# Kernel optimization log

Measured on AMD Instinct MI355X. Metric: run time of the kernel, lower is better.

Reference implementation:

```python
import jax, jax.numpy as jnp
import numpy as np
import math

D_MODEL = 1024
NUM_HEADS = 16
HEAD_DIM = D_MODEL // NUM_HEADS
BATCH = 2
SEQ = 2048
THETA = 10000.0


def _rope_tables(seq_len, head_dim, theta=THETA):
    inv_freq = 1.0 / theta ** (jnp.arange(0, head_dim, 2, dtype=jnp.float32) / head_dim)
    pos = jnp.arange(seq_len, dtype=jnp.float32)
    freqs = jnp.outer(pos, inv_freq)                 # [S, hd/2]
    emb = jnp.concatenate([freqs, freqs], axis=-1)   # [S, hd]
    return jnp.cos(emb), jnp.sin(emb)


def _rotate_half(x):
    x1, x2 = jnp.split(x, 2, axis=-1)
    return jnp.concatenate([-x2, x1], axis=-1)


def setup_inputs() -> dict:
    key = jax.random.key(0)
    k1, k2, k3 = jax.random.split(key, 3)
    x = jax.random.normal(k1, (BATCH, SEQ, D_MODEL), dtype=jnp.float32)
    # causal mask: 1 where attend allowed, 0 where masked
    mask = jnp.tril(jnp.ones((SEQ, SEQ), dtype=jnp.int32))[None, None]
    w_qkv = jax.random.normal(k2, (D_MODEL, 3 * D_MODEL), dtype=jnp.float32) / math.sqrt(D_MODEL)
    w_out = jax.random.normal(k3, (D_MODEL, D_MODEL), dtype=jnp.float32) / math.sqrt(D_MODEL)
    return {"x": x, "mask": mask, "w_qkv": w_qkv, "w_out": w_out}


def reference(x, mask, w_qkv, w_out):
    B, S, _ = x.shape
    qkv = x @ w_qkv                                          # [B,S,3*D]
    qkv = qkv.reshape(B, S, 3, NUM_HEADS, HEAD_DIM)
    qkv = jnp.transpose(qkv, (2, 0, 3, 1, 4))                # [3,B,H,S,hd]
    q, k, v = qkv[0], qkv[1], qkv[2]
    cos, sin = _rope_tables(S, HEAD_DIM)                     # [S,hd]
    cos = cos[None, None]; sin = sin[None, None]
    q = q * cos + _rotate_half(q) * sin
    k = k * cos + _rotate_half(k) * sin
    scores = jnp.einsum('bhqd,bhkd->bhqk', q, k) / math.sqrt(HEAD_DIM)
    scores = jnp.where(mask == 0, -jnp.inf, scores)
    attn = jax.nn.softmax(scores, axis=-1)                   # dropout p=0 (eval)
    out = jnp.einsum('bhqk,bhkd->bhqd', attn, v)             # [B,H,S,hd]
    out = jnp.transpose(out, (0, 2, 1, 3)).reshape(B, S, D_MODEL)
    return out @ w_out
```

## Files before the change

### kernel.cpp

```cpp
#include <hip/hip_runtime.h>

typedef __bf16 bf16;
typedef __bf16 bf16x4 __attribute__((ext_vector_type(4)));
typedef __bf16 bf16x8 __attribute__((ext_vector_type(8)));
typedef short s16x4 __attribute__((ext_vector_type(4)));
typedef float f32x4 __attribute__((ext_vector_type(4)));

constexpr int BATCH = 2;
constexpr int SEQ   = 2048;
constexpr int DMODEL= 1024;
constexpr int NH    = 16;
constexpr int HD    = 64;
constexpr int M_ROWS= BATCH * SEQ;
constexpr int N_QKV = 3 * DMODEL;

#if defined(__HIP_DEVICE_COMPILE__) && __has_builtin(__builtin_amdgcn_exp2f)
#define EXP2(x) __builtin_amdgcn_exp2f(x)
#else
#define EXP2(x) exp2f(x)
#endif

__device__ __forceinline__ void gl_lds16(const bf16* g, bf16* l) {
  __builtin_amdgcn_global_load_lds(
      (const __attribute__((address_space(1))) unsigned int*)g,
      (__attribute__((address_space(3))) unsigned int*)l, 16, 0, 0);
}

__device__ __forceinline__ f32x4 mfma_16x16x16_bf16(bf16x4 a, bf16x4 b,
                                                    f32x4 c) {
#if defined(__HIP_DEVICE_COMPILE__)
  union { bf16x4 h; s16x4 s; } ua{a}, ub{b};
  return __builtin_amdgcn_mfma_f32_16x16x16bf16_1k(ua.s, ub.s, c, 0, 0, 0);
#else
  return c;
#endif
}

__global__ __launch_bounds__(256) void prep_kernel(
    const float* __restrict__ x, const float* __restrict__ w_qkv,
    const float* __restrict__ w_out, bf16* __restrict__ xb,
    bf16* __restrict__ WqkvT, bf16* __restrict__ WoutT) {
  const int bx = blockIdx.x, t = threadIdx.x;
  if (bx < 2048) {
    const int i = (bx * 256 + t) * 8;
    float4 f0 = *(const float4*)&x[i];
    float4 f1 = *(const float4*)&x[i + 4];
    bf16x8 v;
    v[0] = (bf16)f0.x; v[1] = (bf16)f0.y; v[2] = (bf16)f0.z; v[3] = (bf16)f0.w;
    v[4] = (bf16)f1.x; v[5] = (bf16)f1.y; v[6] = (bf16)f1.z; v[7] = (bf16)f1.w;
    *(bf16x8*)&xb[i] = v;
    return;
  }
  __shared__ float tile[32][33];
  const float* src;
  bf16* dst;
  int R, C, c0, r0;
  if (bx < 5120) {
    const int idx = bx - 2048;
    src = w_qkv; dst = WqkvT; R = DMODEL; C = N_QKV;
    c0 = (idx % 96) * 32; r0 = (idx / 96) * 32;
  } else {
    const int idx = bx - 5120;
    src = w_out; dst = WoutT; R = DMODEL; C = DMODEL;
    c0 = (idx & 31) * 32; r0 = (idx >> 5) * 32;
  }
  const int r = t >> 3, c4 = (t & 7) * 4;
  {
    float4 f = *(const float4*)&src[(size_t)(r0 + r) * C + c0 + c4];
    tile[r][c4 + 0] = f.x; tile[r][c4 + 1] = f.y;
    tile[r][c4 + 2] = f.z; tile[r][c4 + 3] = f.w;
  }
  __syncthreads();
  {
    bf16x4 v;
#pragma unroll
    for (int j = 0; j < 4; j++) v[j] = (bf16)tile[c4 + j][r];
    *(bf16x4*)&dst[(size_t)(c0 + r) * R + r0 + c4] = v;
  }
}

__global__ __launch_bounds__(256) void gemm_out64(
    const bf16* __restrict__ A, const bf16* __restrict__ BT,
    float* __restrict__ C, int M, int N, int K) {
  __shared__ bf16 As[64 * 32];
  __shared__ bf16 Bs[128 * 32];
  const int t = threadIdx.x;
  const int m0 = blockIdx.y * 64;
  const int n0 = blockIdx.x * 128;
  const int w = t >> 6, lane = t & 63, g = lane >> 4, li = lane & 15;
  const int r0w = (w & 1) * 32, c0w = (w >> 1) * 64;
  f32x4 acc[2][4] = {};
  for (int k0 = 0; k0 < K; k0 += 32) {
    __syncthreads();
    {
      const int idx = w * 64 + lane;
      const int row = idx >> 2, col = (idx & 3) * 8;
      gl_lds16(&A[(size_t)(m0 + row) * K + k0 + col], &As[w * 512]);
    }
#pragma unroll
    for (int c = 0; c < 2; c++) {
      const int idx = (w * 2 + c) * 64 + lane;
      const int row = idx >> 2, col = (idx & 3) * 8;
      gl_lds16(&BT[(size_t)(n0 + row) * K + k0 + col], &Bs[(w * 2 + c) * 512]);
    }
    __syncthreads();
    bf16x8 a[2], b[4];
#pragma unroll
    for (int mt = 0; mt < 2; mt++)
      a[mt] = *(const bf16x8*)&As[(r0w + mt * 16 + li) * 32 + g * 8];
#pragma unroll
    for (int nt = 0; nt < 4; nt++)
      b[nt] = *(const bf16x8*)&Bs[(c0w + nt * 16 + li) * 32 + g * 8];
#pragma unroll
    for (int mt = 0; mt < 2; mt++)
#pragma unroll
      for (int nt = 0; nt < 4; nt++)
        acc[mt][nt] = __builtin_amdgcn_mfma_f32_16x16x32_bf16(
            a[mt], b[nt], acc[mt][nt], 0, 0, 0);
  }
#pragma unroll
  for (int mt = 0; mt < 2; mt++)
#pragma unroll
    for (int nt = 0; nt < 4; nt++)
#pragma unroll
      for (int r = 0; r < 4; r++) {
        const int m = m0 + r0w + mt * 16 + g * 4 + r;
        const int n = n0 + c0w + nt * 16 + li;
        C[(size_t)m * N + n] = acc[mt][nt][r];
      }
}

__global__ __launch_bounds__(256) void gemm_qkv_rope(
    const bf16* __restrict__ A, const bf16* __restrict__ BT,
    bf16* __restrict__ Qb, bf16* __restrict__ Kb, bf16* __restrict__ Vt) {
  constexpr int K = DMODEL;
  __shared__ bf16 smem[16384];
  const int t = threadIdx.x;
  const int m0 = blockIdx.y * 128;
  const int n0 = blockIdx.x * 128;
  const int w = t >> 6, lane = t & 63, g = lane >> 4, li = lane & 15;
  const int r0w = (w & 1) * 64, c0w = (w >> 1) * 64;
  f32x4 acc[4][4] = {};

  const int i0 = (w * 2 + 0) * 64 + lane, i1 = (w * 2 + 1) * 64 + lane;
  const int sr0 = i0 >> 2, sc0 = (i0 & 3) * 8;
  const int sr1 = i1 >> 2, sc1 = (i1 & 3) * 8;

#define QKV_STAGE(buf, k0)                                                   \
  {                                                                          \
    bf16* Asb = smem + (buf)*4096;                                           \
    bf16* Bsb = smem + 8192 + (buf)*4096;                                    \
    gl_lds16(&A[(size_t)(m0 + sr0) * K + (k0) + sc0],                        \
             &Asb[(w * 2 + 0) * 512]);                                       \
    gl_lds16(&A[(size_t)(m0 + sr1) * K + (k0) + sc1],                        \
             &Asb[(w * 2 + 1) * 512]);                                       \
    gl_lds16(&BT[(size_t)(n0 + sr0) * K + (k0) + sc0],                       \
             &Bsb[(w * 2 + 0) * 512]);                                       \
    gl_lds16(&BT[(size_t)(n0 + sr1) * K + (k0) + sc1],                       \
             &Bsb[(w * 2 + 1) * 512]);                                       \
  }

  QKV_STAGE(0, 0);
  __syncthreads();
  for (int it = 0; it < 32; ++it) {
    const int cur = it & 1;
    if (it < 31) QKV_STAGE(cur ^ 1, (it + 1) * 32);
    const bf16* Asb = smem + cur * 4096;
    const bf16* Bsb = smem + 8192 + cur * 4096;
    bf16x8 a[4], b[4];
#pragma unroll
    for (int mt = 0; mt < 4; mt++)
      a[mt] = *(const bf16x8*)&Asb[(r0w + mt * 16 + li) * 32 + g * 8];
#pragma unroll
    for (int nt = 0; nt < 4; nt++)
      b[nt] = *(const bf16x8*)&Bsb[(c0w + nt * 16 + li) * 32 + g * 8];
#pragma unroll
    for (int mt = 0; mt < 4; mt++)
#pragma unroll
      for (int nt = 0; nt < 4; nt++)
        acc[mt][nt] = __builtin_amdgcn_mfma_f32_16x16x32_bf16(
            a[mt], b[nt], acc[mt][nt], 0, 0, 0);
    __syncthreads();
  }
#undef QKV_STAGE

  const int region = n0 >> 10;
  const int b = m0 >> 11;
  const int h = ((n0 + c0w) >> 6) & 15;
  const size_t bh = (size_t)(b * NH + h);

  if (region < 2) {
    bf16* dst = region == 0 ? Qb : Kb;
    const float outsc = region == 0 ? 0.125f * 1.44269504f : 1.f;
    const float L = 13.287712379549449f;
    const float if0 = exp2f(-(float)(2 * li) / 64.f * L);
    const float if1 = exp2f(-(float)(2 * (li + 16)) / 64.f * L);
    bf16* lw = smem + w * 2112;
#pragma unroll
    for (int pass = 0; pass < 2; pass++) {
      __syncthreads();
#pragma unroll
      for (int mtl = 0; mtl < 2; mtl++) {
        const int mt = pass * 2 + mtl;
#pragma unroll
        for (int r = 0; r < 4; r++) {
          const int s = (m0 + r0w + mt * 16 + g * 4 + r) & (SEQ - 1);
          float cs[2], sn[2];
          __sincosf((float)s * if0, &sn[0], &cs[0]);
          __sincosf((float)s * if1, &sn[1], &cs[1]);
#pragma unroll
          for (int nt = 0; nt < 4; nt++) {
            const int par = nt & 1;
            const float a = acc[mt][nt][r];
            const float ap = acc[mt][nt ^ 2][r];
            const float v = (nt < 2) ? a * cs[par] - ap * sn[par]
                                     : a * cs[par] + ap * sn[par];
            lw[(mtl * 16 + g * 4 + r) * 66 + nt * 16 + li] =
                (bf16)(v * outsc);
          }
        }
      }
      __syncthreads();
      const int rowl = lane >> 1, dh = (lane & 1) * 32;
      const int s = (m0 + r0w + pass * 32 + rowl) & (SEQ - 1);
      bf16* gdst = &dst[(bh * SEQ + s) * HD + dh];
      const bf16* lsrc = &lw[rowl * 66 + dh];
#pragma unroll
      for (int c = 0; c < 4; c++)
        *(bf16x8*)&gdst[c * 8] = *(const bf16x8*)&lsrc[c * 8];
    }
  } else {
#pragma unroll
    for (int mt = 0; mt < 4; mt++)
#pragma unroll
      for (int nt = 0; nt < 4; nt++) {
        const int s = (m0 + r0w + mt * 16 + g * 4) & (SEQ - 1);
        const int d = nt * 16 + li;
        bf16x4 v;
#pragma unroll
        for (int r = 0; r < 4; r++) v[r] = (bf16)acc[mt][nt][r];
        *(bf16x4*)&Vt[(bh * HD + d) * SEQ + s] = v;
      }
  }
}

__device__ const unsigned char CHUNK_TAB[80] = {
    124, 125, 126, 127,
    120, 121, 122, 116, 117, 118, 112, 113, 114, 108, 109, 110,
    104, 105, 106, 100, 101, 102, 96,  97,  98,  92,  93,  94,
    88,  89,  84,  85,  80,  81,  76,  77,  72,  73,  68,  69,
    64,  65,  60,  61,
    56,  52,  48,  44,  40,  36,  32,  28,
    24,  57,  90,  123, 20,  53,  86,  119, 16,  49,  82,  115,
    12,  45,  78,  111, 8,   41,  74,  107, 4,   37,  70,  103,
    0,   33,  66,  99};

__global__ __launch_bounds__(256, 5) void flash_attn15(
    const bf16* __restrict__ Q, const bf16* __restrict__ Kb,
    const bf16* __restrict__ Vt, bf16* __restrict__ Oout,
    float* __restrict__ Opart, float* __restrict__ Lpart) {
  const int bx = blockIdx.x;
  const unsigned char e = CHUNK_TAB[bx >> 5];
  const int qt = e >> 2, kch = e & 3;
  const int bh = bx & 31;
  const int q0 = qt * 64;
  const int jlo = kch * 8;
  const int jhi = min(jlo + 8, qt + 1);
  const int t = threadIdx.x, w = t >> 6, lane = t & 63, g = lane >> 4,
            li = lane & 15;

  __shared__ bf16 Ks[2][4096];
  __shared__ bf16 Vs[2][4096];

  const bf16* Qh = Q  + (size_t)bh * SEQ * HD;
  const bf16* Kh = Kb + (size_t)bh * SEQ * HD;
  const bf16* Vh = Vt + (size_t)bh * HD * SEQ;

  const int qw = q0 + w * 16;

  bf16x8 qf[2];
#pragma unroll
  for (int ks = 0; ks < 2; ks++)
    qf[ks] = *(const bf16x8*)&Qh[(size_t)(qw + li) * HD + ks * 32 + g * 8];

  f32x4 o[4] = {};
  f32x4 o4  = {};
  bf16x4 ones;
#pragma unroll
  for (int r = 0; r < 4; r++) ones[r] = (bf16)1.f;

  int koffB[2][4];
#pragma unroll
  for (int ks = 0; ks < 2; ks++)
#pragma unroll
    for (int nt = 0; nt < 4; nt++) {
      const int rK = nt * 16 + li;
      const int pK = rK * 8 + ((ks * 4 + g) ^ (li & 7));
      koffB[ks][nt] = pK * 16;
    }
  int voffB[4][4];
#pragma unroll
  for (int nt = 0; nt < 4; nt++)
#pragma unroll
    for (int dt = 0; dt < 4; dt++) {
      const int rV = dt * 16 + li;
      const int cg = nt * 2 + (g >> 1);
      const int pV = rV * 8 + (cg ^ (rV & 7));
      voffB[nt][dt] = pV * 16 + (g & 1) * 8;
    }

  const int p0 = w * 128 + lane, p1 = p0 + 64;
  const int sr0 = p0 >> 3, sc0 = ((p0 & 7) ^ (sr0 & 7)) * 8;
  const int sr1 = p1 >> 3, sc1 = ((p1 & 7) ^ (sr1 & 7)) * 8;
  const int lo0 = w * 1024, lo1 = w * 1024 + 512;

  {
    const int jn = jlo * 64;
    gl_lds16(&Kh[(size_t)(jn + sr0) * HD + sc0], &Ks[jlo & 1][lo0]);
    gl_lds16(&Kh[(size_t)(jn + sr1) * HD + sc1], &Ks[jlo & 1][lo1]);
    gl_lds16(&Vh[(size_t)sr0 * SEQ + jn + sc0], &Vs[jlo & 1][lo0]);
    gl_lds16(&Vh[(size_t)sr1 * SEQ + jn + sc1], &Vs[jlo & 1][lo1]);
  }
  __syncthreads();

  for (int ti = jlo; ti < jhi; ++ti) {
    const int cur = ti & 1, nxt = cur ^ 1;
    const char* ksb = (const char*)&Ks[cur][0];
    const char* vsb = (const char*)&Vs[cur][0];
    if (ti + 1 < jhi) {
      const int jn = ti * 64 + 64;
      gl_lds16(&Kh[(size_t)(jn + sr0) * HD + sc0], &Ks[nxt][lo0]);
      gl_lds16(&Kh[(size_t)(jn + sr1) * HD + sc1], &Ks[nxt][lo1]);
      gl_lds16(&Vh[(size_t)sr0 * SEQ + jn + sc0], &Vs[nxt][lo0]);
      gl_lds16(&Vh[(size_t)sr1 * SEQ + jn + sc1], &Vs[nxt][lo1]);
    }

    if (ti < qt) {
      f32x4 sacc[4] = {};
      __builtin_amdgcn_s_setprio(1);
#pragma unroll
      for (int ks = 0; ks < 2; ks++)
#pragma unroll
        for (int nt = 0; nt < 4; nt++) {
          bf16x8 kf = *(const bf16x8*)(ksb + koffB[ks][nt]);
          sacc[nt] = __builtin_amdgcn_mfma_f32_16x16x32_bf16(kf, qf[ks],
                                                             sacc[nt], 0, 0, 0);
        }
      __builtin_amdgcn_s_setprio(0);

      bf16x4 pf[4];
#pragma unroll
      for (int nt = 0; nt < 4; nt++)
#pragma unroll
        for (int r = 0; r < 4; r++) pf[nt][r] = (bf16)EXP2(sacc[nt][r]);

      __builtin_amdgcn_s_setprio(1);
#pragma unroll
      for (int nt = 0; nt < 4; nt++) {
        o4 = mfma_16x16x16_bf16(ones, pf[nt], o4);
#pragma unroll
        for (int dt = 0; dt < 4; dt++) {
          bf16x4 vfrag = *(const bf16x4*)(vsb + voffB[nt][dt]);
          o[dt] = mfma_16x16x16_bf16(vfrag, pf[nt], o[dt]);
        }
      }
      __builtin_amdgcn_s_setprio(0);
    } else {
      f32x4 sacc[4] = {};
      __builtin_amdgcn_s_setprio(1);
#pragma unroll
      for (int ks = 0; ks < 2; ks++)
#pragma unroll
        for (int nt = 0; nt < 4; nt++) {
          if (nt > w) continue;
          bf16x8 kf = *(const bf16x8*)(ksb + koffB[ks][nt]);
          sacc[nt] = __builtin_amdgcn_mfma_f32_16x16x32_bf16(kf, qf[ks],
                                                             sacc[nt], 0, 0, 0);
        }
      __builtin_amdgcn_s_setprio(0);

      bf16x4 pf[4];
#pragma unroll
      for (int nt = 0; nt < 4; nt++) {
        if (nt > w) continue;
#pragma unroll
        for (int r = 0; r < 4; r++) {
          float v = sacc[nt][r];
          if (nt == w) {
            const int kk = nt * 16 + g * 4 + r;
            v = (kk <= w * 16 + li) ? v : -1e30f;
          }
          pf[nt][r] = (bf16)EXP2(v);
        }
      }

      __builtin_amdgcn_s_setprio(1);
#pragma unroll
      for (int nt = 0; nt < 4; nt++) {
        if (nt > w) continue;
        o4 = mfma_16x16x16_bf16(ones, pf[nt], o4);
#pragma unroll
        for (int dt = 0; dt < 4; dt++) {
          bf16x4 vfrag = *(const bf16x4*)(vsb + voffB[nt][dt]);
          o[dt] = mfma_16x16x16_bf16(vfrag, pf[nt], o[dt]);
        }
      }
      __builtin_amdgcn_s_setprio(0);
    }
    __syncthreads();
  }

  if (qt <= 7) {
    const float inv_l = 1.f / o4[0];
    const int b = bh >> 4, h = bh & 15;
    const int s = qw + li;
#pragma unroll
    for (int dt = 0; dt < 4; dt++) {
      bf16x4 ov;
#pragma unroll
      for (int r = 0; r < 4; r++) ov[r] = (bf16)(o[dt][r] * inv_l);
      *(bf16x4*)&Oout[((size_t)(b * SEQ + s)) * DMODEL + h * 64 + dt * 16 +
                      g * 4] = ov;
    }
  } else {
    const int s = qw + li;
    int off;
    if (qt < 16)       off = (s - 512) * 2 + kch;
    else if (qt < 24)  off = 1024 + (s - 1024) * 3 + kch;
    else               off = 2560 + (s - 1536) * 4 + kch;
    const size_t slot = (size_t)bh * 4608 + off;
    if (g == 0) Lpart[slot] = o4[0];
    float* od = &Opart[slot * 64];
#pragma unroll
    for (int dt = 0; dt < 4; dt++)
      *(f32x4*)&od[dt * 16 + g * 4] = o[dt];
  }
}

__global__ __launch_bounds__(256) void attn_merge2(
    const float* __restrict__ Opart, const float* __restrict__ Lpart,
    bf16* __restrict__ attn) {
  const int gi = blockIdx.x * 256 + threadIdx.x;
  const int row = gi >> 3;
  const int d0 = (gi & 7) * 8;
  const int bh = row / 1536, srel = row - bh * 1536;
  const int b = bh >> 4, h = bh & 15, s = srel + 512;
  int off0, nc;
  if (srel < 512)       { off0 = srel * 2;                nc = 2; }
  else if (srel < 1024) { off0 = 1024 + (srel - 512) * 3; nc = 3; }
  else                  { off0 = 2560 + (srel - 1024) * 4; nc = 4; }
  const size_t base = (size_t)bh * 4608 + off0;
  float lsum = 0.f;
  float acc[8] = {};
  for (int c = 0; c < nc; c++) {
    lsum += Lpart[base + c];
    const float* p = &Opart[(base + c) * 64 + d0];
    float4 a0 = *(const float4*)p;
    float4 a1 = *(const float4*)(p + 4);
    acc[0] += a0.x; acc[1] += a0.y; acc[2] += a0.z; acc[3] += a0.w;
    acc[4] += a1.x; acc[5] += a1.y; acc[6] += a1.z; acc[7] += a1.w;
  }
  const float inv = 1.f / lsum;
  bf16x8 v;
#pragma unroll
  for (int i = 0; i < 8; i++) v[i] = (bf16)(acc[i] * inv);
  *(bf16x8*)&attn[((size_t)(b * SEQ + s)) * DMODEL + h * 64 + d0] = v;
}

extern "C" void kernel_launch(void* const* d_in, const int* in_sizes, int n_in,
                              void* d_out, int out_size, void* d_ws,
                              size_t ws_size, hipStream_t stream) {
  const float* x     = (const float*)d_in[0];
  const float* w_qkv = (const float*)d_in[2];
  const float* w_out = (const float*)d_in[3];
  float* out = (float*)d_out;

  char* ws = (char*)d_ws;
  bf16* WqkvT = (bf16*)(ws);
  bf16* WoutT = (bf16*)(ws + 6291456);
  bf16* xb    = (bf16*)(ws + 8388608);
  bf16* Qb    = (bf16*)(ws + 16777216);
  bf16* Kbuf  = (bf16*)(ws + 25165824);
  bf16* Vt    = (bf16*)(ws + 33554432);
  bf16* attn  = (bf16*)(ws + 41943040);
  float* Opart= (float*)(ws + 50331648);
  float* Lpart= (float*)(ws + 88080384);

  prep_kernel<<<dim3(6144), 256, 0, stream>>>(x, w_qkv, w_out, xb, WqkvT,
                                              WoutT);
  gemm_qkv_rope<<<dim3(N_QKV / 128, M_ROWS / 128), 256, 0, stream>>>(
      xb, WqkvT, Qb, Kbuf, Vt);
  flash_attn15<<<dim3(2560), 256, 0, stream>>>(Qb, Kbuf, Vt, attn, Opart,
                                               Lpart);
  attn_merge2<<<dim3(1536), 256, 0, stream>>>(Opart, Lpart, attn);
  gemm_out64<<<dim3(DMODEL / 128, M_ROWS / 64), 256, 0, stream>>>(
      attn, WoutT, out, M_ROWS, DMODEL, DMODEL);
}
```

Baseline: 198.5 us.

## Fuse split-KV merge into flash attention via atomic ticket last-block reduction

Removes the separate attn_merge2 kernel. Each split-KV attention block now writes its partials, fences, and takes an atomic ticket per (head, q-tile); the last-arriving block sums the Lpart/Opart partials and writes the normalized bf16 output. The ticket counters are zeroed by an extra block in prep_kernel. This saves a kernel launch and lets the merge overlap with other attention blocks, at the cost of atomics, fences and a serialized tail reduction inside the attention kernel.

```diff
diff --git a/kernel.cpp b/kernel.cpp
--- a/kernel.cpp
+++ b/kernel.cpp
@@ -39,7 +39,8 @@
 __global__ __launch_bounds__(256) void prep_kernel(
     const float* __restrict__ x, const float* __restrict__ w_qkv,
     const float* __restrict__ w_out, bf16* __restrict__ xb,
-    bf16* __restrict__ WqkvT, bf16* __restrict__ WoutT) {
+    bf16* __restrict__ WqkvT, bf16* __restrict__ WoutT,
+    int* __restrict__ ticket) {
   const int bx = blockIdx.x, t = threadIdx.x;
   if (bx < 2048) {
     const int i = (bx * 256 + t) * 8;
@@ -49,6 +50,11 @@
     v[0] = (bf16)f0.x; v[1] = (bf16)f0.y; v[2] = (bf16)f0.z; v[3] = (bf16)f0.w;
     v[4] = (bf16)f1.x; v[5] = (bf16)f1.y; v[6] = (bf16)f1.z; v[7] = (bf16)f1.w;
     *(bf16x8*)&xb[i] = v;
+    return;
+  }
+  if (bx >= 6144) {
+    int4 z = {0, 0, 0, 0};
+    *(int4*)&ticket[t * 4] = z;
     return;
   }
   __shared__ float tile[32][33];
@@ -255,10 +261,11 @@
     12,  45,  78,  111, 8,   41,  74,  107, 4,   37,  70,  103,
     0,   33,  66,  99};
 
-__global__ __launch_bounds__(256, 5) void flash_attn15(
+__global__ __launch_bounds__(256, 5) void flash_attn16(
     const bf16* __restrict__ Q, const bf16* __restrict__ Kb,
     const bf16* __restrict__ Vt, bf16* __restrict__ Oout,
-    float* __restrict__ Opart, float* __restrict__ Lpart) {
+    float* __restrict__ Opart, float* __restrict__ Lpart,
+    int* __restrict__ ticket) {
   const int bx = blockIdx.x;
   const unsigned char e = CHUNK_TAB[bx >> 5];
   const int qt = e >> 2, kch = e & 3;
@@ -434,37 +441,48 @@
 #pragma unroll
     for (int dt = 0; dt < 4; dt++)
       *(f32x4*)&od[dt * 16 + g * 4] = o[dt];
-  }
-}
-
-__global__ __launch_bounds__(256) void attn_merge2(
-    const float* __restrict__ Opart, const float* __restrict__ Lpart,
-    bf16* __restrict__ attn) {
-  const int gi = blockIdx.x * 256 + threadIdx.x;
-  const int row = gi >> 3;
-  const int d0 = (gi & 7) * 8;
-  const int bh = row / 1536, srel = row - bh * 1536;
-  const int b = bh >> 4, h = bh & 15, s = srel + 512;
-  int off0, nc;
-  if (srel < 512)       { off0 = srel * 2;                nc = 2; }
-  else if (srel < 1024) { off0 = 1024 + (srel - 512) * 3; nc = 3; }
-  else                  { off0 = 2560 + (srel - 1024) * 4; nc = 4; }
-  const size_t base = (size_t)bh * 4608 + off0;
-  float lsum = 0.f;
-  float acc[8] = {};
-  for (int c = 0; c < nc; c++) {
-    lsum += Lpart[base + c];
-    const float* p = &Opart[(base + c) * 64 + d0];
-    float4 a0 = *(const float4*)p;
-    float4 a1 = *(const float4*)(p + 4);
-    acc[0] += a0.x; acc[1] += a0.y; acc[2] += a0.z; acc[3] += a0.w;
-    acc[4] += a1.x; acc[5] += a1.y; acc[6] += a1.z; acc[7] += a1.w;
-  }
-  const float inv = 1.f / lsum;
-  bf16x8 v;
-#pragma unroll
-  for (int i = 0; i < 8; i++) v[i] = (bf16)(acc[i] * inv);
-  *(bf16x8*)&attn[((size_t)(b * SEQ + s)) * DMODEL + h * 64 + d0] = v;
+
+    __threadfence();
+    __syncthreads();
+    volatile int* flag = (volatile int*)&Ks[0][0];
+    if (t == 0)
+      *flag = (atomicAdd(&ticket[bh * 32 + qt], 1) == (qt >> 3)) ? 1 : 0;
+    __syncthreads();
+    if (*flag) {
+      __threadfence();
+      const int nc = (qt >> 3) + 1;
+      const int b = bh >> 4, h = bh & 15;
+      const int row = t >> 2;
+      const int srow = q0 + row;
+      int off0;
+      if (qt < 16)       off0 = (srow - 512) * 2;
+      else if (qt < 24)  off0 = 1024 + (srow - 1024) * 3;
+      else               off0 = 2560 + (srow - 1536) * 4;
+      const size_t base2 = (size_t)bh * 4608 + off0;
+      float lsum = 0.f;
+      for (int c = 0; c < nc; c++) lsum += Lpart[base2 + c];
+      const float inv = 1.f / lsum;
+      const int d0 = (t & 3) * 16;
+      float am[16] = {};
+      for (int c = 0; c < nc; c++) {
+        const float* p = &Opart[(base2 + c) * 64 + d0];
+#pragma unroll
+        for (int i = 0; i < 16; i += 4) {
+          float4 f = *(const float4*)(p + i);
+          am[i] += f.x; am[i + 1] += f.y; am[i + 2] += f.z; am[i + 3] += f.w;
+        }
+      }
+      bf16x8 v0, v1;
+#pragma unroll
+      for (int i = 0; i < 8; i++) {
+        v0[i] = (bf16)(am[i] * inv);
+        v1[i] = (bf16)(am[8 + i] * inv);
+      }
+      bf16* gp = &Oout[((size_t)(b * SEQ + srow)) * DMODEL + h * 64 + d0];
+      *(bf16x8*)gp = v0;
+      *(bf16x8*)(gp + 8) = v1;
+    }
+  }
 }
 
 extern "C" void kernel_launch(void* const* d_in, const int* in_sizes, int n_in,
@@ -485,14 +503,14 @@
   bf16* attn  = (bf16*)(ws + 41943040);
   float* Opart= (float*)(ws + 50331648);
   float* Lpart= (float*)(ws + 88080384);
-
-  prep_kernel<<<dim3(6144), 256, 0, stream>>>(x, w_qkv, w_out, xb, WqkvT,
-                                              WoutT);
+  int*  ticket= (int*)(ws + 88670208);
+
+  prep_kernel<<<dim3(6145), 256, 0, stream>>>(x, w_qkv, w_out, xb, WqkvT,
+                                              WoutT, ticket);
   gemm_qkv_rope<<<dim3(N_QKV / 128, M_ROWS / 128), 256, 0, stream>>>(
       xb, WqkvT, Qb, Kbuf, Vt);
-  flash_attn15<<<dim3(2560), 256, 0, stream>>>(Qb, Kbuf, Vt, attn, Opart,
-                                               Lpart);
-  attn_merge2<<<dim3(1536), 256, 0, stream>>>(Opart, Lpart, attn);
+  flash_attn16<<<dim3(2560), 256, 0, stream>>>(Qb, Kbuf, Vt, attn, Opart,
+                                               Lpart, ticket);
   gemm_out64<<<dim3(DMODEL / 128, M_ROWS / 64), 256, 0, stream>>>(
       attn, WoutT, out, M_ROWS, DMODEL, DMODEL);
 }
```

After: 567.3 us. 186% more time.
